# Kernel optimization log

Measured on AMD Instinct MI355X. Metric: run time of the kernel, lower is better.

The kernel has to match this reference:

```python
import jax, jax.numpy as jnp
import numpy as np

T, B, IN, H, L, C = 512, 4096, 12, 32, 10, 4


def setup_inputs() -> dict:
    key = jax.random.key(0)
    ks = jax.random.split(key, 12)
    s = 1.0 / np.sqrt(H)  # PyTorch GRU init scale ~ U(-1/sqrt(H), 1/sqrt(H))
    return {
        "x": jax.random.normal(ks[0], (T, B, IN), jnp.float32),
        "W_ih0": jax.random.normal(ks[1], (3 * H, IN), jnp.float32) * s,
        "W_hh0": jax.random.normal(ks[2], (3 * H, H), jnp.float32) * s,
        "b_ih0": jax.random.normal(ks[3], (3 * H,), jnp.float32) * s,
        "b_hh0": jax.random.normal(ks[4], (3 * H,), jnp.float32) * s,
        "W_ih": jax.random.normal(ks[5], (L - 1, 3 * H, H), jnp.float32) * s,
        "W_hh": jax.random.normal(ks[6], (L - 1, 3 * H, H), jnp.float32) * s,
        "b_ih": jax.random.normal(ks[7], (L - 1, 3 * H), jnp.float32) * s,
        "b_hh": jax.random.normal(ks[8], (L - 1, 3 * H), jnp.float32) * s,
        "fc_W": jax.random.normal(ks[9], (C, H), jnp.float32) * s,
        "fc_b": jax.random.normal(ks[10], (C,), jnp.float32) * s,
        "lengths": jax.random.randint(ks[11], (B,), 1, T + 1, jnp.int32),
    }


def gru_cell(x_t, h, Wi, Wh, bi, bh):
    # PyTorch GRU cell math
    gi = x_t @ Wi.T + bi          # [B, 3H]
    gh = h @ Wh.T + bh            # [B, 3H]
    i_r, i_z, i_n = jnp.split(gi, 3, axis=-1)
    h_r, h_z, h_n = jnp.split(gh, 3, axis=-1)
    r = jax.nn.sigmoid(i_r + h_r)
    z = jax.nn.sigmoid(i_z + h_z)
    n = jnp.tanh(i_n + r * h_n)
    return (1.0 - z) * n + z * h


def reference(x, W_ih0, W_hh0, b_ih0, b_hh0, W_ih, W_hh, b_ih, b_hh, fc_W, fc_b, lengths):
    Bn = x.shape[1]
    h0 = jnp.zeros((L, Bn, H), x.dtype)

    def step(h, x_t):
        hs = []
        inp = x_t
        for l in range(L):
            if l == 0:
                hl = gru_cell(inp, h[0], W_ih0, W_hh0, b_ih0, b_hh0)
            else:
                hl = gru_cell(inp, h[l], W_ih[l - 1], W_hh[l - 1], b_ih[l - 1], b_hh[l - 1])
            hs.append(hl)
            inp = hl
        return jnp.stack(hs), inp  # carry all-layer hidden, emit top-layer output

    _, outs = jax.lax.scan(step, h0, x)  # [T, B, H]
    idx = jnp.maximum(lengths, 1) - 1    # last valid timestep per sequence
    last = outs[idx, jnp.arange(Bn)]     # [B, H]
    logits = last @ fc_W.T + fc_b        # [B, C]
    return jax.nn.log_softmax(logits, axis=1)
```

## Files before the change

### kernel.cpp

```cpp
#include <hip/hip_runtime.h>
#include <math.h>

#define TT 512
#define BB 4096
#define IN_DIM 12
#define HH 32
#define LL 10
#define CC 4
#define NTH (LL * 64)

typedef _Float16 half8 __attribute__((ext_vector_type(8)));
typedef _Float16 half4 __attribute__((ext_vector_type(4)));
typedef float f32x4 __attribute__((ext_vector_type(4)));

#define LOG2E 1.44269504088896340736f

#define H_HI 0
#define H_LO (LL * 4 * 512)
#define X_HI (H_LO + LL * 2 * 512)
#define LDS16_TOT (X_HI + 2 * 512)

#define MFMA_(A, B, C) C = __builtin_amdgcn_mfma_f32_16x16x32_f16(A, B, C, 0, 0, 0)

__global__ __launch_bounds__(NTH, 2)
void gru_fused_mfma(const float* __restrict__ x,
                    const float* __restrict__ Wih0,
                    const float* __restrict__ Whh0,
                    const float* __restrict__ bih0,
                    const float* __restrict__ bhh0,
                    const float* __restrict__ Wih,
                    const float* __restrict__ Whh,
                    const float* __restrict__ bih,
                    const float* __restrict__ bhh,
                    const int*   __restrict__ lengths,
                    float*       __restrict__ last)
{
    __shared__ __align__(16) _Float16 lds16[LDS16_TOT];
    __shared__ int flagS[LL];
    __shared__ int rflagS[LL];

    const int tid  = threadIdx.x;
    const int w    = tid >> 6;
    const int lane = tid & 63;
    const int bi16 = lane & 15;
    const int quad = lane >> 4;
    const int bg   = blockIdx.x;

    {
        float4 z4 = make_float4(0.f, 0.f, 0.f, 0.f);
        float4* p = (float4*)lds16;
        for (int i = tid; i < LDS16_TOT / 8; i += NTH) p[i] = z4;
    }
    if (lane == 0) { flagS[w] = -1; rflagS[w] = -1; }
    __syncthreads();

    const float *Wi, *Wh, *bivec, *bhvec;
    int wistride;
    if (w == 0) { Wi = Wih0; Wh = Whh0; bivec = bih0; bhvec = bhh0; wistride = IN_DIM; }
    else {
        Wi = Wih + (size_t)(w - 1) * 96 * HH;
        Wh = Whh + (size_t)(w - 1) * 96 * HH;
        bivec = bih + (size_t)(w - 1) * 96;
        bhvec = bhh + (size_t)(w - 1) * 96;
        wistride = HH;
    }

    const int frow[12] = {0, 0, 16, 16, 32, 32, 48, 48, 64, 80, 64, 80};
    const int fchk[12] = {0, 1, 0, 1, 0, 1, 0, 1, 0, 0, 1, 1};
    half8 Whi[12], Wlo[6];
#pragma unroll
    for (int f = 0; f < 12; f++) {
        const float sc = (f < 8) ? -LOG2E : 2.0f * LOG2E;
        int row = frow[f] + bi16;
        const float* src; int kin;
        if (fchk[f] == 0) { src = Wi + (size_t)row * wistride; kin = wistride; }
        else              { src = Wh + (size_t)row * HH;       kin = HH; }
        int wloidx = (f < 8) ? (f >> 1) : (f - 6);
#pragma unroll
        for (int kk = 0; kk < 8; kk++) {
            int k = quad * 8 + kk;
            float v = (k < kin) ? src[k] * sc : 0.0f;
            _Float16 h = (_Float16)v;
            Whi[f][kk] = h;
            if (fchk[f] == 1) Wlo[wloidx][kk] = (_Float16)(v - (float)h);
        }
    }

    f32x4 biasreg[8];
#pragma unroll
    for (int ct = 0; ct < 8; ct++) {
        int g = ct >> 1, jt = ct & 1;
#pragma unroll
        for (int r = 0; r < 4; r++) {
            int j = jt * 16 + quad * 4 + r;
            float v;
            if      (g == 0) v = -(bivec[j]      + bhvec[j])      * LOG2E;
            else if (g == 1) v = -(bivec[32 + j] + bhvec[32 + j]) * LOG2E;
            else if (g == 2) v = bivec[64 + j] * (2.0f * LOG2E);
            else             v = bhvec[64 + j] * (2.0f * LOG2E);
            biasreg[ct][r] = v;
        }
    }

    int capT = -1;
    if (w == LL - 1) {
        int len = lengths[bg * 16 + bi16];
        capT = ((len < 1) ? 1 : len) - 1;
    }

    const int laneoff = lane * 8;
    const int inbase  = (w == 0) ? X_HI : (H_HI + (w - 1) * 2048);
    const int inmask  = (w == 0) ? 1 : 3;
    const int ownhi   = H_HI + w * 2048;
    const int ownlo   = H_LO + w * 1024;
    const int wibase  = (quad >> 1) * 128 + bi16 * 8 + (quad & 1) * 4;

    const int xbb = lane / 3, xkg = lane - xbb * 3;
    const int xq   = (xkg == 2) ? 1 : 0;
    const int xoff = (xkg == 1) ? 4 : 0;
    const int xidx = xq * 128 + xbb * 8 + xoff;
    const bool xlane = (w == 0) && (lane < 48);

    auto stage_x = [&](const float4& xl, int t) {
        half4 h4;
        h4[0] = (_Float16)xl.x; h4[1] = (_Float16)xl.y;
        h4[2] = (_Float16)xl.z; h4[3] = (_Float16)xl.w;
        *(half4*)(lds16 + X_HI + ((t & 1) << 9) + xidx) = h4;
    };

    if (xlane) {
        float4 x0 = *(const float4*)(x + (size_t)bg * 192 + lane * 4);
        float4 x1 = *(const float4*)(x + (size_t)BB * IN_DIM + (size_t)bg * 192 + lane * 4);
        stage_x(x0, 0);
        stage_x(x1, 1);
    }

    float hprev[8] = {0, 0, 0, 0, 0, 0, 0, 0};
    __syncthreads();

    auto substep = [&](int t) {
        half8 bxh = *(const half8*)(lds16 + inbase + ((t & inmask) << 9) + laneoff);
        half8 bhh = *(const half8*)(lds16 + ownhi + (((t + 3) & 3) << 9) + laneoff);
        half8 bhl = *(const half8*)(lds16 + ownlo + (((t + 1) & 1) << 9) + laneoff);

        f32x4 acc[8];
#pragma unroll
        for (int ct = 0; ct < 8; ct++) acc[ct] = biasreg[ct];

#pragma unroll
        for (int ct = 0; ct < 4; ct++) {
            MFMA_(Whi[ct * 2 + 0], bxh, acc[ct]);
            MFMA_(Whi[ct * 2 + 1], bhh, acc[ct]);
            MFMA_(Whi[ct * 2 + 1], bhl, acc[ct]);
            MFMA_(Wlo[ct],         bhh, acc[ct]);
        }
#pragma unroll
        for (int jt = 0; jt < 2; jt++) {
            MFMA_(Whi[8 + jt],  bxh, acc[4 + jt]);
            MFMA_(Whi[10 + jt], bhh, acc[6 + jt]);
            MFMA_(Whi[10 + jt], bhl, acc[6 + jt]);
            MFMA_(Wlo[4 + jt],  bhh, acc[6 + jt]);
        }

#pragma unroll
        for (int jt = 0; jt < 2; jt++) {
            f32x4 R = acc[0 + jt], Z = acc[2 + jt];
            f32x4 IN_ = acc[4 + jt], HN = acc[6 + jt];
            half4 h4, l4;
            float hv[4];
#pragma unroll
            for (int r = 0; r < 4; r++) {
                float rv = __builtin_amdgcn_rcpf(1.0f + __builtin_amdgcn_exp2f(R[r]));
                float zv = __builtin_amdgcn_rcpf(1.0f + __builtin_amdgcn_exp2f(Z[r]));
                float ea = __builtin_amdgcn_exp2f(fmaf(rv, HN[r], IN_[r]));
                float nv = fmaf(-2.0f, __builtin_amdgcn_rcpf(ea + 1.0f), 1.0f);
                float h  = fmaf(zv, hprev[jt * 4 + r] - nv, nv);
                hprev[jt * 4 + r] = h;
                _Float16 hh16 = (_Float16)h;
                h4[r] = hh16;
                l4[r] = (_Float16)(h - (float)hh16);
                hv[r] = h;
            }
            int wi = jt * 256 + wibase;
            *(half4*)(lds16 + ownhi + ((t & 3) << 9) + wi) = h4;
            *(half4*)(lds16 + ownlo + ((t & 1) << 9) + wi) = l4;
            if (w == LL - 1 && t == capT) {
                float4 o = make_float4(hv[0], hv[1], hv[2], hv[3]);
                *(float4*)(last + (size_t)(bg * 16 + bi16) * HH + jt * 16 + quad * 4) = o;
            }
        }
    };

    for (int t = 0; t < TT; t += 2) {
        if (w > 0) {
            while (__hip_atomic_load(&flagS[w - 1], __ATOMIC_ACQUIRE,
                                     __HIP_MEMORY_SCOPE_WORKGROUP) < t + 1)
                __builtin_amdgcn_s_sleep(1);
        }
        if (w < LL - 1) {
            while (__hip_atomic_load(&rflagS[w], __ATOMIC_ACQUIRE,
                                     __HIP_MEMORY_SCOPE_WORKGROUP) < t - 3)
                __builtin_amdgcn_s_sleep(1);
        }

        float4 xa0, xa1;
        bool dl0 = false, dl1 = false;
        if (xlane) {
            if (t + 2 < TT) {
                xa0 = *(const float4*)(x + (size_t)(t + 2) * BB * IN_DIM +
                                       (size_t)bg * 192 + lane * 4);
                dl0 = true;
            }
            if (t + 3 < TT) {
                xa1 = *(const float4*)(x + (size_t)(t + 3) * BB * IN_DIM +
                                       (size_t)bg * 192 + lane * 4);
                dl1 = true;
            }
        }

        substep(t);
        substep(t + 1);

        if (dl0) stage_x(xa0, t + 2);
        if (dl1) stage_x(xa1, t + 3);

        if (lane == 0) {
            if (w < LL - 1)
                __hip_atomic_store(&flagS[w], t + 1, __ATOMIC_RELEASE,
                                   __HIP_MEMORY_SCOPE_WORKGROUP);
            if (w > 0)
                __hip_atomic_store(&rflagS[w - 1], t + 1, __ATOMIC_RELEASE,
                                   __HIP_MEMORY_SCOPE_WORKGROUP);
        }
    }
}

__global__ __launch_bounds__(256)
void fc_head(const float* __restrict__ last,
             const float* __restrict__ fcW,
             const float* __restrict__ fcb,
             float* __restrict__ out)
{
    int b = blockIdx.x * blockDim.x + threadIdx.x;
    if (b >= BB) return;
    float lg[CC];
#pragma unroll
    for (int c = 0; c < CC; c++) lg[c] = fcb[c];
#pragma unroll
    for (int j = 0; j < HH; j++) {
        float h = last[(size_t)b * HH + j];
#pragma unroll
        for (int c = 0; c < CC; c++) lg[c] = fmaf(fcW[c * HH + j], h, lg[c]);
    }
    float m = lg[0];
#pragma unroll
    for (int c = 1; c < CC; c++) m = fmaxf(m, lg[c]);
    float s = 0.0f;
#pragma unroll
    for (int c = 0; c < CC; c++) s += __expf(lg[c] - m);
    float lse = m + logf(s);
#pragma unroll
    for (int c = 0; c < CC; c++) out[(size_t)b * CC + c] = lg[c] - lse;
}

extern "C" void kernel_launch(void* const* d_in, const int* in_sizes, int n_in,
                              void* d_out, int out_size, void* d_ws, size_t ws_size,
                              hipStream_t stream)
{
    const float* x    = (const float*)d_in[0];
    const float* Wih0 = (const float*)d_in[1];
    const float* Whh0 = (const float*)d_in[2];
    const float* bih0 = (const float*)d_in[3];
    const float* bhh0 = (const float*)d_in[4];
    const float* Wih  = (const float*)d_in[5];
    const float* Whh  = (const float*)d_in[6];
    const float* bih  = (const float*)d_in[7];
    const float* bhh  = (const float*)d_in[8];
    const float* fcW  = (const float*)d_in[9];
    const float* fcb  = (const float*)d_in[10];
    const int*   lens = (const int*)d_in[11];
    float* out = (float*)d_out;

    float* last = (float*)d_ws;

    gru_fused_mfma<<<dim3(BB / 16), dim3(NTH), 0, stream>>>(
        x, Wih0, Whh0, bih0, bhh0, Wih, Whh, bih, bhh, lens, last);

    fc_head<<<dim3(BB / 256), dim3(256), 0, stream>>>(last, fcW, fcb, out);
}
```

Baseline: 962.4 us.

## Deepen layer ring buffers, fold bias into MFMA, pack gate math, share reciprocals

```diff
diff --git a/kernel.cpp b/kernel.cpp
--- a/kernel.cpp
+++ b/kernel.cpp
@@ -12,13 +12,14 @@
 typedef _Float16 half8 __attribute__((ext_vector_type(8)));
 typedef _Float16 half4 __attribute__((ext_vector_type(4)));
 typedef float f32x4 __attribute__((ext_vector_type(4)));
+typedef float f32x2 __attribute__((ext_vector_type(2)));
 
 #define LOG2E 1.44269504088896340736f
 
 #define H_HI 0
-#define H_LO (LL * 4 * 512)
+#define H_LO (LL * 8 * 512)
 #define X_HI (H_LO + LL * 2 * 512)
-#define LDS16_TOT (X_HI + 2 * 512)
+#define LDS16_TOT (X_HI + 4 * 512)
 
 #define MFMA_(A, B, C) C = __builtin_amdgcn_mfma_f32_16x16x32_f16(A, B, C, 0, 0, 0)
 
@@ -109,9 +110,9 @@
     }
 
     const int laneoff = lane * 8;
-    const int inbase  = (w == 0) ? X_HI : (H_HI + (w - 1) * 2048);
-    const int inmask  = (w == 0) ? 1 : 3;
-    const int ownhi   = H_HI + w * 2048;
+    const int inbase  = (w == 0) ? X_HI : (H_HI + (w - 1) * 4096);
+    const int inmask  = (w == 0) ? 3 : 7;
+    const int ownhi   = H_HI + w * 4096;
     const int ownlo   = H_LO + w * 1024;
     const int wibase  = (quad >> 1) * 128 + bi16 * 8 + (quad & 1) * 4;
 
@@ -125,7 +126,7 @@
         half4 h4;
         h4[0] = (_Float16)xl.x; h4[1] = (_Float16)xl.y;
         h4[2] = (_Float16)xl.z; h4[3] = (_Float16)xl.w;
-        *(half4*)(lds16 + X_HI + ((t & 1) << 9) + xidx) = h4;
+        *(half4*)(lds16 + X_HI + ((t & 3) << 9) + xidx) = h4;
     };
 
     if (xlane) {
@@ -135,54 +136,86 @@
         stage_x(x1, 1);
     }
 
-    float hprev[8] = {0, 0, 0, 0, 0, 0, 0, 0};
+    f32x2 hprev[4];
+#pragma unroll
+    for (int i = 0; i < 4; i++) { hprev[i][0] = 0.0f; hprev[i][1] = 0.0f; }
+
     __syncthreads();
 
     auto substep = [&](int t) {
         half8 bxh = *(const half8*)(lds16 + inbase + ((t & inmask) << 9) + laneoff);
-        half8 bhh = *(const half8*)(lds16 + ownhi + (((t + 3) & 3) << 9) + laneoff);
+        half8 bhh = *(const half8*)(lds16 + ownhi + (((t + 7) & 7) << 9) + laneoff);
         half8 bhl = *(const half8*)(lds16 + ownlo + (((t + 1) & 1) << 9) + laneoff);
 
         f32x4 acc[8];
-#pragma unroll
-        for (int ct = 0; ct < 8; ct++) acc[ct] = biasreg[ct];
-
+
+        __builtin_amdgcn_s_setprio(1);
 #pragma unroll
         for (int ct = 0; ct < 4; ct++) {
-            MFMA_(Whi[ct * 2 + 0], bxh, acc[ct]);
+            acc[ct] = __builtin_amdgcn_mfma_f32_16x16x32_f16(
+                          Whi[ct * 2 + 0], bxh, biasreg[ct], 0, 0, 0);
             MFMA_(Whi[ct * 2 + 1], bhh, acc[ct]);
             MFMA_(Whi[ct * 2 + 1], bhl, acc[ct]);
             MFMA_(Wlo[ct],         bhh, acc[ct]);
         }
 #pragma unroll
         for (int jt = 0; jt < 2; jt++) {
-            MFMA_(Whi[8 + jt],  bxh, acc[4 + jt]);
-            MFMA_(Whi[10 + jt], bhh, acc[6 + jt]);
+            acc[4 + jt] = __builtin_amdgcn_mfma_f32_16x16x32_f16(
+                              Whi[8 + jt], bxh, biasreg[4 + jt], 0, 0, 0);
+            acc[6 + jt] = __builtin_amdgcn_mfma_f32_16x16x32_f16(
+                              Whi[10 + jt], bhh, biasreg[6 + jt], 0, 0, 0);
             MFMA_(Whi[10 + jt], bhl, acc[6 + jt]);
             MFMA_(Wlo[4 + jt],  bhh, acc[6 + jt]);
         }
+        __builtin_amdgcn_s_setprio(0);
 
 #pragma unroll
         for (int jt = 0; jt < 2; jt++) {
-            f32x4 R = acc[0 + jt], Z = acc[2 + jt];
-            f32x4 IN_ = acc[4 + jt], HN = acc[6 + jt];
             half4 h4, l4;
             float hv[4];
 #pragma unroll
-            for (int r = 0; r < 4; r++) {
-                float rv = __builtin_amdgcn_rcpf(1.0f + __builtin_amdgcn_exp2f(R[r]));
-                float zv = __builtin_amdgcn_rcpf(1.0f + __builtin_amdgcn_exp2f(Z[r]));
-                float ea = __builtin_amdgcn_exp2f(fmaf(rv, HN[r], IN_[r]));
-                float nv = fmaf(-2.0f, __builtin_amdgcn_rcpf(ea + 1.0f), 1.0f);
-                float h  = fmaf(zv, hprev[jt * 4 + r] - nv, nv);
-                hprev[jt * 4 + r] = h;
-                _Float16 hh16 = (_Float16)h;
-                h4[r] = hh16;
-                l4[r] = (_Float16)(h - (float)hh16);
-                hv[r] = h;
+            for (int pr = 0; pr < 2; pr++) {
+                f32x2 R2, Z2, I2, H2;
+                R2[0] = acc[0 + jt][2 * pr]; R2[1] = acc[0 + jt][2 * pr + 1];
+                Z2[0] = acc[2 + jt][2 * pr]; Z2[1] = acc[2 + jt][2 * pr + 1];
+                I2[0] = acc[4 + jt][2 * pr]; I2[1] = acc[4 + jt][2 * pr + 1];
+                H2[0] = acc[6 + jt][2 * pr]; H2[1] = acc[6 + jt][2 * pr + 1];
+                f32x2 av, bv;
+                av[0] = __builtin_amdgcn_exp2f(R2[0]);
+                av[1] = __builtin_amdgcn_exp2f(R2[1]);
+                bv[0] = __builtin_amdgcn_exp2f(Z2[0]);
+                bv[1] = __builtin_amdgcn_exp2f(Z2[1]);
+                av = av + 1.0f;
+                bv = bv + 1.0f;
+                f32x2 pv = av * bv;
+                float q  = __builtin_amdgcn_rcpf(pv[0] * pv[1]);
+                f32x2 qs; qs[0] = q * pv[1]; qs[1] = q * pv[0];
+                f32x2 rv = qs * bv;
+                f32x2 zv = qs * av;
+                f32x2 na = __builtin_elementwise_fma(rv, H2, I2);
+                f32x2 ea;
+                ea[0] = __builtin_amdgcn_exp2f(na[0]);
+                ea[1] = __builtin_amdgcn_exp2f(na[1]);
+                f32x2 dv = ea + 1.0f;
+                float qn = __builtin_amdgcn_rcpf(dv[0] * dv[1]);
+                f32x2 qv; qv[0] = qn * dv[1]; qv[1] = qn * dv[0];
+                f32x2 m2; m2[0] = -2.0f; m2[1] = -2.0f;
+                f32x2 o1; o1[0] = 1.0f;  o1[1] = 1.0f;
+                f32x2 nv = __builtin_elementwise_fma(m2, qv, o1);
+                f32x2 hp = hprev[jt * 2 + pr];
+                f32x2 hn = __builtin_elementwise_fma(zv, hp - nv, nv);
+                hprev[jt * 2 + pr] = hn;
+                _Float16 hh0 = (_Float16)hn[0], hh1 = (_Float16)hn[1];
+                f32x2 hi32; hi32[0] = (float)hh0; hi32[1] = (float)hh1;
+                f32x2 lo2 = hn - hi32;
+                h4[2 * pr]     = hh0; h4[2 * pr + 1] = hh1;
+                l4[2 * pr]     = (_Float16)lo2[0];
+                l4[2 * pr + 1] = (_Float16)lo2[1];
+                hv[2 * pr]     = hn[0];
+                hv[2 * pr + 1] = hn[1];
             }
             int wi = jt * 256 + wibase;
-            *(half4*)(lds16 + ownhi + ((t & 3) << 9) + wi) = h4;
+            *(half4*)(lds16 + ownhi + ((t & 7) << 9) + wi) = h4;
             *(half4*)(lds16 + ownlo + ((t & 1) << 9) + wi) = l4;
             if (w == LL - 1 && t == capT) {
                 float4 o = make_float4(hv[0], hv[1], hv[2], hv[3]);
@@ -199,7 +232,7 @@
         }
         if (w < LL - 1) {
             while (__hip_atomic_load(&rflagS[w], __ATOMIC_ACQUIRE,
-                                     __HIP_MEMORY_SCOPE_WORKGROUP) < t - 3)
+                                     __HIP_MEMORY_SCOPE_WORKGROUP) < t - 7)
                 __builtin_amdgcn_s_sleep(1);
         }
 
```

New measurement: 1.011 ms. 5.0% more time.
